# Kernel optimization log

Hardware: AMD Instinct MI355X
Metric: run time of the kernel (lower is better)

## Reference

```python
import jax, jax.numpy as jnp
import numpy as np

# Static multi-scale pyramid (H, W per level); Nv = sum(H*W) = 13294
SPATIAL = np.array([[100, 100], [50, 50], [25, 25], [13, 13]], dtype=np.int64)
B, C, NH, NL, NP = 2, 256, 8, 4, 4
D = C // NH
TOT = NH * NL * NP


def setup_inputs() -> dict:
    key = jax.random.key(0)
    ks = jax.random.split(key, 10)
    Nv = int((SPATIAL[:, 0] * SPATIAL[:, 1]).sum())
    Nq = Nv
    query = jax.random.normal(ks[0], (B, Nq, C), dtype=jnp.float32)
    value = jax.random.normal(ks[1], (B, Nv, C), dtype=jnp.float32)
    reference_points = jax.random.uniform(ks[2], (B, Nq, NL, 2), minval=0.05, maxval=0.95, dtype=jnp.float32)
    spatial_shapes = jnp.asarray(SPATIAL)
    level_start_index = jnp.asarray(np.concatenate([[0], np.cumsum(SPATIAL[:, 0] * SPATIAL[:, 1])[:-1]]))
    # sampling_offsets: small random weight + the rotated-grid bias from _reset_parameters
    W_off = 0.01 * jax.random.normal(ks[3], (C, TOT * 2), dtype=jnp.float32)
    thetas = np.arange(NH, dtype=np.float64) * (2.0 * np.pi / NH)
    grid = np.stack([np.cos(thetas), np.sin(thetas)], -1)
    grid = grid / np.abs(grid).max(-1, keepdims=True)
    grid = np.tile(grid[:, None, None, :], (1, NL, NP, 1)) * (np.arange(NP) + 1)[None, None, :, None]
    b_off = jnp.asarray(grid.reshape(-1), dtype=jnp.float32)
    W_attn = 0.01 * jax.random.normal(ks[4], (C, TOT), dtype=jnp.float32)
    b_attn = jnp.zeros((TOT,), jnp.float32)
    W_val = jax.random.normal(ks[5], (C, C), dtype=jnp.float32) / np.sqrt(C)
    b_val = jnp.zeros((C,), jnp.float32)
    W_out = jax.random.normal(ks[6], (C, C), dtype=jnp.float32) / np.sqrt(C)
    b_out = jnp.zeros((C,), jnp.float32)
    return {"query": query, "value": value, "reference_points": reference_points,
            "spatial_shapes": spatial_shapes, "level_start_index": level_start_index,
            "W_off": W_off, "b_off": b_off, "W_attn": W_attn, "b_attn": b_attn,
            "W_val": W_val, "b_val": b_val, "W_out": W_out, "b_out": b_out}


def _bilinear(vl, loc, H, W):
    # vl: [B, h, H*W, D]; loc: [B, Nq, h, P, 2] normalized (x, y) in [0,1]
    # Matches F.grid_sample(mode='bilinear', padding_mode='zeros', align_corners=False)
    Bb, h, _, Dd = vl.shape
    Nq, P = loc.shape[1], loc.shape[3]
    x = loc[..., 0] * W - 0.5
    y = loc[..., 1] * H - 0.5
    x0 = jnp.floor(x)
    y0 = jnp.floor(y)
    fx = x - x0
    fy = y - y0
    out = jnp.zeros((Bb, h, Nq * P, Dd), vl.dtype)
    corners = ((0, 0, (1 - fx) * (1 - fy)), (1, 0, fx * (1 - fy)),
               (0, 1, (1 - fx) * fy), (1, 1, fx * fy))
    for dx, dy, w in corners:
        xi = x0 + dx
        yi = y0 + dy
        valid = (xi >= 0) & (xi < W) & (yi >= 0) & (yi < H)
        idx = (jnp.clip(yi, 0, H - 1) * W + jnp.clip(xi, 0, W - 1)).astype(jnp.int32)
        idx = idx.transpose(0, 2, 1, 3).reshape(Bb, h, Nq * P)          # [B,h,Nq*P]
        wv = (w * valid).transpose(0, 2, 1, 3).reshape(Bb, h, Nq * P)   # [B,h,Nq*P]
        g = jnp.take_along_axis(vl, idx[..., None], axis=2)             # [B,h,Nq*P,D]
        out = out + g * wv[..., None]
    return out.reshape(Bb, h, Nq, P, Dd)


def reference(query, value, reference_points, spatial_shapes, level_start_index,
              W_off, b_off, W_attn, b_attn, W_val, b_val, W_out, b_out):
    Bb, Nq, Cc = query.shape
    v = (value @ W_val + b_val).reshape(Bb, -1, NH, D)                  # [B,Nv,h,D]
    off = (query @ W_off + b_off).reshape(Bb, Nq, NH, NL, NP, 2)
    attn = jax.nn.softmax((query @ W_attn + b_attn).reshape(Bb, Nq, NH, NL * NP), axis=-1)
    attn = attn.reshape(Bb, Nq, NH, NL, NP)
    # offset normalizer is (W, H) per level
    norm = jnp.asarray(SPATIAL[:, ::-1].copy(), dtype=query.dtype)      # [L,2]
    loc = reference_points[:, :, None, :, None, :] + off / norm[None, None, None, :, None, :]
    starts = np.concatenate([[0], np.cumsum(SPATIAL[:, 0] * SPATIAL[:, 1])])
    out_acc = jnp.zeros((Bb, NH, Nq, D), query.dtype)
    for l in range(NL):
        H, W = int(SPATIAL[l, 0]), int(SPATIAL[l, 1])
        vl = v[:, int(starts[l]):int(starts[l + 1])].transpose(0, 2, 1, 3)  # [B,h,HW,D]
        samp = _bilinear(vl, loc[:, :, :, l], H, W)                     # [B,h,Nq,P,D]
        w_l = attn[:, :, :, l].transpose(0, 2, 1, 3)                    # [B,h,Nq,P]
        out_acc = out_acc + jnp.einsum('bhqpd,bhqp->bhqd', samp, w_l)
    out = out_acc.transpose(0, 2, 1, 3).reshape(Bb, Nq, Cc)
    return out @ W_out + b_out
```

## Files before the change

kernel.cpp:

```cpp
#include <hip/hip_runtime.h>
#include <hip/hip_bf16.h>

#define NQ  13294
#define NV  13294
#define BQ  26588

typedef __attribute__((ext_vector_type(8))) short short8;
typedef __attribute__((ext_vector_type(4))) float f32x4;

static __device__ __forceinline__ ushort f2bf(float f) {
    unsigned int x = __float_as_uint(f);
    unsigned int r = (x + 0x7fffu + ((x >> 16) & 1u)) >> 16;
    return (ushort)r;
}
static __device__ __forceinline__ uint cvtpk_bf16(float a, float b) {
    uint r;
    asm("v_cvt_pk_bf16_f32 %0, %1, %2" : "=v"(r) : "v"(a), "v"(b));
    return r;
}
static __device__ __forceinline__ uint cvtpk_f16(float a, float b) {
    uint r;
    asm("v_cvt_pkrtz_f16_f32 %0, %1, %2" : "=v"(r) : "v"(a), "v"(b));
    return r;
}
static __device__ __forceinline__ float f16lo(uint u) {
    _Float16 h; ushort t = (ushort)(u & 0xffffu);
    __builtin_memcpy(&h, &t, 2); return (float)h;
}
static __device__ __forceinline__ float f16hi(uint u) {
    _Float16 h; ushort t = (ushort)(u >> 16);
    __builtin_memcpy(&h, &t, 2); return (float)h;
}
static __device__ __forceinline__ float fmamix_ll(float acc, uint g, uint w) {
    asm("v_fma_mix_f32 %0, %1, %2, %0 op_sel:[0,0,0] op_sel_hi:[1,1,0]" : "+v"(acc) : "v"(g), "v"(w));
    return acc;
}
static __device__ __forceinline__ float fmamix_hl(float acc, uint g, uint w) {
    asm("v_fma_mix_f32 %0, %1, %2, %0 op_sel:[1,0,0] op_sel_hi:[1,1,0]" : "+v"(acc) : "v"(g), "v"(w));
    return acc;
}
static __device__ __forceinline__ float fmamix_lh(float acc, uint g, uint w) {
    asm("v_fma_mix_f32 %0, %1, %2, %0 op_sel:[0,1,0] op_sel_hi:[1,1,0]" : "+v"(acc) : "v"(g), "v"(w));
    return acc;
}
static __device__ __forceinline__ float fmamix_hh(float acc, uint g, uint w) {
    asm("v_fma_mix_f32 %0, %1, %2, %0 op_sel:[1,1,0] op_sel_hi:[1,1,0]" : "+v"(acc) : "v"(g), "v"(w));
    return acc;
}

__global__ __launch_bounds__(256) void prep_weights(
    const float* __restrict__ Wv, const float* __restrict__ Wo,
    const float* __restrict__ Wa, const float* __restrict__ Wu,
    const float* __restrict__ bo, const float* __restrict__ ba,
    ushort* __restrict__ tWv, ushort* __restrict__ tWoa,
    ushort* __restrict__ tWu, float* __restrict__ boa) {
    const int blk = blockIdx.x;
    const int tid = threadIdx.x;
    if (blk == 56) {
        if (tid < 256) boa[tid] = bo[tid];
        int j = tid + 256;
        if (j < 384) boa[j] = ba[j - 256];
        return;
    }
    __shared__ float t[64][65];
    const float* src; ushort* dst; int srcN, k0, n0, drow0;
    if (blk < 16)      { int u = blk;      src = Wv; srcN = 256; dst = tWv;  k0 = (u >> 2) * 64; n0 = (u & 3) * 64; drow0 = n0; }
    else if (blk < 32) { int u = blk - 16; src = Wo; srcN = 256; dst = tWoa; k0 = (u >> 2) * 64; n0 = (u & 3) * 64; drow0 = n0; }
    else if (blk < 40) { int u = blk - 32; src = Wa; srcN = 128; dst = tWoa; k0 = (u >> 1) * 64; n0 = (u & 1) * 64; drow0 = 256 + n0; }
    else               { int u = blk - 40; src = Wu; srcN = 256; dst = tWu;  k0 = (u >> 2) * 64; n0 = (u & 3) * 64; drow0 = n0; }
#pragma unroll
    for (int it = 0; it < 16; ++it) {
        int idx = tid + it * 256, r = idx >> 6, c = idx & 63;
        t[r][c] = src[(size_t)(k0 + r) * srcN + n0 + c];
    }
    __syncthreads();
#pragma unroll
    for (int it = 0; it < 16; ++it) {
        int idx = tid + it * 256, r = idx >> 6, c = idx & 63;
        dst[(size_t)(drow0 + r) * 256 + k0 + c] = f2bf(t[c][r]);
    }
}

#define LDP 40

template<int AF32>
static __device__ __forceinline__ void gemm_core(
    const void* __restrict__ Aptr, const ushort* __restrict__ Bt,
    const float* __restrict__ bias, void* __restrict__ Cout,
    int M, int N, int out_mode, int mblk, int nblk,
    ushort* sA, ushort* sB) {
    const int tid = threadIdx.x;
    const int wid = tid >> 6;
    const int lane = tid & 63;
    const int row0 = mblk * 128;
    const int col0 = nblk * 128;
    const int wr = (wid >> 1) * 64;
    const int wc = (wid & 1) * 64;

    f32x4 acc[4][4];
#pragma unroll
    for (int m = 0; m < 4; ++m)
#pragma unroll
        for (int n = 0; n < 4; ++n) acc[m][n] = (f32x4){0.f, 0.f, 0.f, 0.f};

    for (int kk = 0; kk < 256; kk += 32) {
        __syncthreads();
#pragma unroll
        for (int it = 0; it < 2; ++it) {
            int chunk = tid + it * 256;
            int r = chunk >> 2;
            int seg = chunk & 3;
            int gr = row0 + r; gr = gr < M ? gr : M - 1;
            uint4 wa;
            if (AF32) {
                const float* Af = (const float*)Aptr + (size_t)gr * 256 + kk + seg * 8;
                float4 f0 = *reinterpret_cast<const float4*>(Af);
                float4 f1 = *reinterpret_cast<const float4*>(Af + 4);
                wa.x = cvtpk_bf16(f0.x, f0.y);
                wa.y = cvtpk_bf16(f0.z, f0.w);
                wa.z = cvtpk_bf16(f1.x, f1.y);
                wa.w = cvtpk_bf16(f1.z, f1.w);
            } else {
                wa = *reinterpret_cast<const uint4*>((const ushort*)Aptr + (size_t)gr * 256 + kk + seg * 8);
            }
            *reinterpret_cast<uint4*>(&sA[r * LDP + seg * 8]) = wa;
            int gc = col0 + r;
            uint4 vb4 = *reinterpret_cast<const uint4*>(Bt + (size_t)gc * 256 + kk + seg * 8);
            *reinterpret_cast<uint4*>(&sB[r * LDP + seg * 8]) = vb4;
        }
        __syncthreads();

        short8 a[4], b[4];
#pragma unroll
        for (int m = 0; m < 4; ++m)
            a[m] = *reinterpret_cast<const short8*>(&sA[(wr + m * 16 + (lane & 15)) * LDP + (lane >> 4) * 8]);
#pragma unroll
        for (int n = 0; n < 4; ++n)
            b[n] = *reinterpret_cast<const short8*>(&sB[(wc + n * 16 + (lane & 15)) * LDP + (lane >> 4) * 8]);
#pragma unroll
        for (int m = 0; m < 4; ++m)
#pragma unroll
            for (int n = 0; n < 4; ++n)
                acc[m][n] = __builtin_amdgcn_mfma_f32_16x16x32_bf16(a[m], b[n], acc[m][n], 0, 0, 0);
    }

    const int lr = (lane >> 4) * 4;
    const int lc = lane & 15;
#pragma unroll
    for (int m = 0; m < 4; ++m) {
#pragma unroll
        for (int n = 0; n < 4; ++n) {
            int gcol = col0 + wc + n * 16 + lc;
            float bv = bias[gcol];
#pragma unroll
            for (int j = 0; j < 4; ++j) {
                int grow = row0 + wr + m * 16 + lr + j;
                if (grow < M) {
                    float vv = acc[m][n][j] + bv;
                    if (out_mode == 0) {
                        ((float*)Cout)[(size_t)grow * N + gcol] = vv;
                    } else if (out_mode == 2) {
                        ((ushort*)Cout)[(size_t)grow * N + gcol] = (ushort)(cvtpk_f16(vv, vv) & 0xffffu);
                    } else {
                        int bb = grow >= NV;
                        int pix = grow - bb * NV;
                        int h = gcol >> 5, ch = gcol & 31;
                        ((ushort*)Cout)[(((size_t)(bb * 8 + h)) * NV + pix) * 32 + ch] =
                            (ushort)(cvtpk_f16(vv, vv) & 0xffffu);
                    }
                }
            }
        }
    }
}

__global__ __launch_bounds__(256) void gemm_fused(
    const float* __restrict__ value, const float* __restrict__ query,
    const ushort* __restrict__ tWv, const ushort* __restrict__ tWoa,
    const float* __restrict__ bval, const float* __restrict__ boa,
    ushort* __restrict__ vproj_t, ushort* __restrict__ offattn) {
    __shared__ ushort sA[128 * LDP];
    __shared__ ushort sB[128 * LDP];
    const bool g1 = blockIdx.y < 2;
    gemm_core<1>(g1 ? (const void*)value : (const void*)query,
                 g1 ? tWv : tWoa, g1 ? bval : boa,
                 g1 ? (void*)vproj_t : (void*)offattn,
                 BQ, g1 ? 256 : 384, g1 ? 3 : 2,
                 blockIdx.x, g1 ? blockIdx.y : blockIdx.y - 2, sA, sB);
}

__global__ __launch_bounds__(256) void gemm_out(
    const ushort* __restrict__ outacc, const ushort* __restrict__ tWu,
    const float* __restrict__ bout, float* __restrict__ dout) {
    __shared__ ushort sA[128 * LDP];
    __shared__ ushort sB[128 * LDP];
    gemm_core<0>(outacc, tWu, bout, dout, BQ, 256, 0, blockIdx.x, blockIdx.y, sA, sB);
}

__global__ __launch_bounds__(256, 4) void msda_sample(
    const ushort* __restrict__ offattn,
    const float* __restrict__ refp,
    const ushort* __restrict__ vt,
    ushort* __restrict__ out_acc) {
    __shared__ int2 s_ad[4][256];
    __shared__ uint s_w[4][256];

    const int tid = threadIdx.x;
    const int qi = tid >> 6;
    const int lane = tid & 63;
    const int bq = blockIdx.x * 4 + qi;
    const int b = bq / NQ;
    const int q = bq - b * NQ;
    const int h = lane >> 3;

    const ushort* oa = offattn + (size_t)bq * 384;
    const int t0 = lane * 2;
    uint lgu = *reinterpret_cast<const uint*>(oa + 256 + t0);
    float lg0 = f16lo(lgu), lg1 = f16hi(lgu);
    float m = fmaxf(lg0, lg1);
    m = fmaxf(m, __shfl_xor(m, 1));
    m = fmaxf(m, __shfl_xor(m, 2));
    m = fmaxf(m, __shfl_xor(m, 4));
    float e0 = __expf(lg0 - m), e1 = __expf(lg1 - m);
    float ssum = e0 + e1;
    ssum += __shfl_xor(ssum, 1);
    ssum += __shfl_xor(ssum, 2);
    ssum += __shfl_xor(ssum, 4);
    float inv = 1.f / ssum;

    uint2 offu = *reinterpret_cast<const uint2*>(oa + 2 * t0);
    const int l = (t0 >> 2) & 3;
    const int   Wi = (l == 0) ? 100 : (l == 1) ? 50 : (l == 2) ? 25 : 13;
    const int   st = (l == 0) ? 0 : (l == 1) ? 10000 : (l == 2) ? 12500 : 13125;
    const float Wf = (float)Wi;
    float rx = refp[(((size_t)b * NQ + q) * 4 + l) * 2 + 0];
    float ry = refp[(((size_t)b * NQ + q) * 4 + l) * 2 + 1];
    const int vbase = (b * 8 + h) * NV * 64;

#pragma unroll
    for (int j = 0; j < 2; ++j) {
        float e = (j ? e1 : e0) * inv;
        float ox = j ? f16lo(offu.y) : f16lo(offu.x);
        float oy = j ? f16hi(offu.y) : f16hi(offu.x);
        float x = fmaf(rx, Wf, ox) - 0.5f;
        float y = fmaf(ry, Wf, oy) - 0.5f;
        float x0f = floorf(x), y0f = floorf(y);
        float fx = x - x0f, fy = y - y0f;
        int x0 = (int)x0f, y0 = (int)y0f;
        float wx0 = (x0 >= 0 && x0 < Wi)         ? e * (1.f - fx) : 0.f;
        float wx1 = (x0 + 1 >= 0 && x0 + 1 < Wi) ? e * fx         : 0.f;
        float wy0 = (y0 >= 0 && y0 < Wi)         ? (1.f - fy) : 0.f;
        float wy1 = (y0 + 1 >= 0 && y0 + 1 < Wi) ? fy         : 0.f;
        int px0 = min(max(x0, 0), Wi - 1) * 64;
        int px1 = min(max(x0 + 1, 0), Wi - 1) * 64;
        int a0 = vbase + (st + min(max(y0, 0), Wi - 1) * Wi) * 64;
        int a1 = vbase + (st + min(max(y0 + 1, 0), Wi - 1) * Wi) * 64;
        int s = 2 * (lane & 7) + j;
        int u = ((s ^ h) << 4) + (h << 1);
        s_ad[qi][u]     = make_int2(a0 + px0, a1 + px0);
        s_ad[qi][u + 1] = make_int2(a0 + px1, a1 + px1);
        s_w[qi][u]      = cvtpk_f16(wx0 * wy0, wx0 * wy1);
        s_w[qi][u + 1]  = cvtpk_f16(wx1 * wy0, wx1 * wy1);
    }
    __syncthreads();

    const int xbit = (lane >> 2) & 1;
    const int cg16 = (lane & 3) * 16;
    const char* vtc = (const char*)vt;

    int2 A[16]; uint Wp[16];
#pragma unroll
    for (int ss = 0; ss < 16; ++ss) {
        int u = ((ss ^ h) << 4) + (h << 1) + xbit;
        int2 a = s_ad[qi][u];
        A[ss] = make_int2(a.x + cg16, a.y + cg16);
        Wp[ss] = s_w[qi][u];
    }

    float acc[8] = {0.f, 0.f, 0.f, 0.f, 0.f, 0.f, 0.f, 0.f};
#pragma unroll
    for (int ss = 0; ss < 16; ++ss) {
        uint4 g0 = *reinterpret_cast<const uint4*>(vtc + (uint)A[ss].x);
        uint4 g1 = *reinterpret_cast<const uint4*>(vtc + (uint)A[ss].y);
        uint w = Wp[ss];
        acc[0] = fmamix_ll(acc[0], g0.x, w); acc[1] = fmamix_hl(acc[1], g0.x, w);
        acc[2] = fmamix_ll(acc[2], g0.y, w); acc[3] = fmamix_hl(acc[3], g0.y, w);
        acc[4] = fmamix_ll(acc[4], g0.z, w); acc[5] = fmamix_hl(acc[5], g0.z, w);
        acc[6] = fmamix_ll(acc[6], g0.w, w); acc[7] = fmamix_hl(acc[7], g0.w, w);
        acc[0] = fmamix_lh(acc[0], g1.x, w); acc[1] = fmamix_hh(acc[1], g1.x, w);
        acc[2] = fmamix_lh(acc[2], g1.y, w); acc[3] = fmamix_hh(acc[3], g1.y, w);
        acc[4] = fmamix_lh(acc[4], g1.z, w); acc[5] = fmamix_hh(acc[5], g1.z, w);
        acc[6] = fmamix_lh(acc[6], g1.w, w); acc[7] = fmamix_hh(acc[7], g1.w, w);
    }

#pragma unroll
    for (int i = 0; i < 8; ++i) acc[i] += __shfl_xor(acc[i], 4);
    if (xbit == 0) {
        uint4 o;
        o.x = cvtpk_bf16(acc[0], acc[1]);
        o.y = cvtpk_bf16(acc[2], acc[3]);
        o.z = cvtpk_bf16(acc[4], acc[5]);
        o.w = cvtpk_bf16(acc[6], acc[7]);
        *reinterpret_cast<uint4*>(out_acc + (size_t)bq * 256 + h * 32 + (lane & 3) * 8) = o;
    }
}

extern "C" void kernel_launch(void* const* d_in, const int* in_sizes, int n_in,
                              void* d_out, int out_size, void* d_ws, size_t ws_size,
                              hipStream_t stream) {
    const float* query  = (const float*)d_in[0];
    const float* value  = (const float*)d_in[1];
    const float* refp   = (const float*)d_in[2];
    const float* W_off  = (const float*)d_in[5];
    const float* b_off  = (const float*)d_in[6];
    const float* W_attn = (const float*)d_in[7];
    const float* b_attn = (const float*)d_in[8];
    const float* W_val  = (const float*)d_in[9];
    const float* b_val  = (const float*)d_in[10];
    const float* W_out  = (const float*)d_in[11];
    const float* b_out  = (const float*)d_in[12];

    const size_t ROWB = (size_t)BQ * 256 * 2;
    char* ws = (char*)d_ws;
    ushort* vproj_t = (ushort*)(ws);
    ushort* outacc  = (ushort*)(ws + ROWB);
    ushort* offattn = (ushort*)(ws + 2 * ROWB);
    char*   wbase   = ws + 2 * ROWB + (size_t)BQ * 384 * 2;
    ushort* tWv  = (ushort*)(wbase);
    ushort* tWoa = tWv + 65536;
    ushort* tWu  = tWoa + 98304;
    float*  boa  = (float*)(tWu + 65536);

    prep_weights<<<57, 256, 0, stream>>>(
        W_val, W_off, W_attn, W_out, b_off, b_attn, tWv, tWoa, tWu, boa);

    gemm_fused<<<dim3(208, 5), 256, 0, stream>>>(
        value, query, tWv, tWoa, b_val, boa, vproj_t, offattn);

    msda_sample<<<BQ / 4, 256, 0, stream>>>(offattn, refp, vproj_t, outacc);

    gemm_out<<<dim3(208, 2), 256, 0, stream>>>(outacc, tWu, b_out, (float*)d_out);
}
```

Baseline: 107.9 us.

## Double-buffer GEMM shared-memory tiles with register prefetch of next K slice

The GEMM core now loads the next 32-wide K slice from global memory into registers while MFMAs run on the current shared-memory buffer. It then writes that slice into the alternate buffer, so each K step needs one barrier instead of two. This is meant to hide global-load latency behind compute in the projection GEMMs. In exchange it doubles LDS use per block, holds more prefetch registers, and adds a launch-bounds occupancy hint of 3 blocks per CU.

```diff
diff --git a/kernel.cpp b/kernel.cpp
--- a/kernel.cpp
+++ b/kernel.cpp
@@ -82,9 +82,10 @@
 }
 
 #define LDP 40
+#define ABUF (128 * LDP)
 
 template<int AF32>
-static __device__ __forceinline__ void gemm_core(
+static __device__ __forceinline__ void gemm_core2(
     const void* __restrict__ Aptr, const ushort* __restrict__ Bt,
     const float* __restrict__ bias, void* __restrict__ Cout,
     int M, int N, int out_mode, int mblk, int nblk,
@@ -103,45 +104,69 @@
 #pragma unroll
         for (int n = 0; n < 4; ++n) acc[m][n] = (f32x4){0.f, 0.f, 0.f, 0.f};
 
-    for (int kk = 0; kk < 256; kk += 32) {
-        __syncthreads();
+    const int r0 = tid >> 2;
+    const int seg = tid & 3;
+
+    float4 rf[4];
+    uint4  ra[2];
+    uint4  rb[2];
+
+    auto REGLOAD = [&](int kk) {
 #pragma unroll
         for (int it = 0; it < 2; ++it) {
-            int chunk = tid + it * 256;
-            int r = chunk >> 2;
-            int seg = chunk & 3;
+            int r = r0 + it * 64;
             int gr = row0 + r; gr = gr < M ? gr : M - 1;
+            if (AF32) {
+                const float* Af = (const float*)Aptr + (size_t)gr * 256 + kk + seg * 8;
+                rf[2 * it]     = *reinterpret_cast<const float4*>(Af);
+                rf[2 * it + 1] = *reinterpret_cast<const float4*>(Af + 4);
+            } else {
+                ra[it] = *reinterpret_cast<const uint4*>((const ushort*)Aptr + (size_t)gr * 256 + kk + seg * 8);
+            }
+            int gc = col0 + r;
+            rb[it] = *reinterpret_cast<const uint4*>(Bt + (size_t)gc * 256 + kk + seg * 8);
+        }
+    };
+    auto STORE = [&](int buf) {
+#pragma unroll
+        for (int it = 0; it < 2; ++it) {
+            int r = r0 + it * 64;
             uint4 wa;
             if (AF32) {
-                const float* Af = (const float*)Aptr + (size_t)gr * 256 + kk + seg * 8;
-                float4 f0 = *reinterpret_cast<const float4*>(Af);
-                float4 f1 = *reinterpret_cast<const float4*>(Af + 4);
-                wa.x = cvtpk_bf16(f0.x, f0.y);
-                wa.y = cvtpk_bf16(f0.z, f0.w);
-                wa.z = cvtpk_bf16(f1.x, f1.y);
-                wa.w = cvtpk_bf16(f1.z, f1.w);
+                wa.x = cvtpk_bf16(rf[2 * it].x, rf[2 * it].y);
+                wa.y = cvtpk_bf16(rf[2 * it].z, rf[2 * it].w);
+                wa.z = cvtpk_bf16(rf[2 * it + 1].x, rf[2 * it + 1].y);
+                wa.w = cvtpk_bf16(rf[2 * it + 1].z, rf[2 * it + 1].w);
             } else {
-                wa = *reinterpret_cast<const uint4*>((const ushort*)Aptr + (size_t)gr * 256 + kk + seg * 8);
+                wa = ra[it];
             }
-            *reinterpret_cast<uint4*>(&sA[r * LDP + seg * 8]) = wa;
-            int gc = col0 + r;
-            uint4 vb4 = *reinterpret_cast<const uint4*>(Bt + (size_t)gc * 256 + kk + seg * 8);
-            *reinterpret_cast<uint4*>(&sB[r * LDP + seg * 8]) = vb4;
+            *reinterpret_cast<uint4*>(&sA[buf * ABUF + r * LDP + seg * 8]) = wa;
+            *reinterpret_cast<uint4*>(&sB[buf * ABUF + r * LDP + seg * 8]) = rb[it];
         }
-        __syncthreads();
-
+    };
+    auto COMPUTE = [&](int buf) {
         short8 a[4], b[4];
 #pragma unroll
         for (int m = 0; m < 4; ++m)
-            a[m] = *reinterpret_cast<const short8*>(&sA[(wr + m * 16 + (lane & 15)) * LDP + (lane >> 4) * 8]);
+            a[m] = *reinterpret_cast<const short8*>(&sA[buf * ABUF + (wr + m * 16 + (lane & 15)) * LDP + (lane >> 4) * 8]);
 #pragma unroll
         for (int n = 0; n < 4; ++n)
-            b[n] = *reinterpret_cast<const short8*>(&sB[(wc + n * 16 + (lane & 15)) * LDP + (lane >> 4) * 8]);
+            b[n] = *reinterpret_cast<const short8*>(&sB[buf * ABUF + (wc + n * 16 + (lane & 15)) * LDP + (lane >> 4) * 8]);
 #pragma unroll
         for (int m = 0; m < 4; ++m)
 #pragma unroll
             for (int n = 0; n < 4; ++n)
                 acc[m][n] = __builtin_amdgcn_mfma_f32_16x16x32_bf16(a[m], b[n], acc[m][n], 0, 0, 0);
+    };
+
+    REGLOAD(0);
+    STORE(0);
+#pragma unroll
+    for (int t = 0; t < 8; ++t) {
+        __syncthreads();
+        if (t < 7) REGLOAD((t + 1) * 32);
+        COMPUTE(t & 1);
+        if (t < 7) STORE((t + 1) & 1);
     }
 
     const int lr = (lane >> 4) * 4;
@@ -174,27 +199,27 @@
     }
 }
 
-__global__ __launch_bounds__(256) void gemm_fused(
+__global__ __launch_bounds__(256, 3) void gemm_fused(
     const float* __restrict__ value, const float* __restrict__ query,
     const ushort* __restrict__ tWv, const ushort* __restrict__ tWoa,
     const float* __restrict__ bval, const float* __restrict__ boa,
     ushort* __restrict__ vproj_t, ushort* __restrict__ offattn) {
-    __shared__ ushort sA[128 * LDP];
-    __shared__ ushort sB[128 * LDP];
+    __shared__ ushort sA[2 * ABUF];
+    __shared__ ushort sB[2 * ABUF];
     const bool g1 = blockIdx.y < 2;
-    gemm_core<1>(g1 ? (const void*)value : (const void*)query,
-                 g1 ? tWv : tWoa, g1 ? bval : boa,
-                 g1 ? (void*)vproj_t : (void*)offattn,
-                 BQ, g1 ? 256 : 384, g1 ? 3 : 2,
-                 blockIdx.x, g1 ? blockIdx.y : blockIdx.y - 2, sA, sB);
-}
-
-__global__ __launch_bounds__(256) void gemm_out(
+    gemm_core2<1>(g1 ? (const void*)value : (const void*)query,
+                  g1 ? tWv : tWoa, g1 ? bval : boa,
+                  g1 ? (void*)vproj_t : (void*)offattn,
+                  BQ, g1 ? 256 : 384, g1 ? 3 : 2,
+                  blockIdx.x, g1 ? blockIdx.y : blockIdx.y - 2, sA, sB);
+}
+
+__global__ __launch_bounds__(256, 3) void gemm_out(
     const ushort* __restrict__ outacc, const ushort* __restrict__ tWu,
     const float* __restrict__ bout, float* __restrict__ dout) {
-    __shared__ ushort sA[128 * LDP];
-    __shared__ ushort sB[128 * LDP];
-    gemm_core<0>(outacc, tWu, bout, dout, BQ, 256, 0, blockIdx.x, blockIdx.y, sA, sB);
+    __shared__ ushort sA[2 * ABUF];
+    __shared__ ushort sB[2 * ABUF];
+    gemm_core2<0>(outacc, tWu, bout, dout, BQ, 256, 0, blockIdx.x, blockIdx.y, sA, sB);
 }
 
 __global__ __launch_bounds__(256, 4) void msda_sample(
```

Result: no change. 107.8 us (-0.0%).

## Keep full-K A row panel resident in LDS and loop over N blocks

Applied to the files above, without the earlier changes.

GEMMs now load a 128-row A panel for the whole K=256 into shared memory once (converting fp32 to bf16 once) and iterate over all N column blocks inside one block. B tiles are register-prefetched one K step ahead. This removes repeated global reads and conversions of A across column blocks, at the cost of fewer blocks, larger dynamic LDS per block and serialized N work.

```diff
diff --git a/kernel.cpp b/kernel.cpp
--- a/kernel.cpp
+++ b/kernel.cpp
@@ -7,6 +7,10 @@
 
 typedef __attribute__((ext_vector_type(8))) short short8;
 typedef __attribute__((ext_vector_type(4))) float f32x4;
+
+#define ALD 264
+#define BLD 40
+#define LDS_USH (128 * ALD + 128 * BLD)
 
 static __device__ __forceinline__ ushort f2bf(float f) {
     unsigned int x = __float_as_uint(f);
@@ -81,92 +85,109 @@
     }
 }
 
-#define LDP 40
-
 template<int AF32>
-static __device__ __forceinline__ void gemm_core(
+static __device__ __forceinline__ void gemm_rowres(
     const void* __restrict__ Aptr, const ushort* __restrict__ Bt,
     const float* __restrict__ bias, void* __restrict__ Cout,
-    int M, int N, int out_mode, int mblk, int nblk,
-    ushort* sA, ushort* sB) {
+    int M, int N, int out_mode, int mblk, ushort* sA, ushort* sB) {
     const int tid = threadIdx.x;
     const int wid = tid >> 6;
     const int lane = tid & 63;
     const int row0 = mblk * 128;
-    const int col0 = nblk * 128;
     const int wr = (wid >> 1) * 64;
     const int wc = (wid & 1) * 64;
 
-    f32x4 acc[4][4];
-#pragma unroll
-    for (int m = 0; m < 4; ++m)
-#pragma unroll
-        for (int n = 0; n < 4; ++n) acc[m][n] = (f32x4){0.f, 0.f, 0.f, 0.f};
-
-    for (int kk = 0; kk < 256; kk += 32) {
-        __syncthreads();
-#pragma unroll
-        for (int it = 0; it < 2; ++it) {
-            int chunk = tid + it * 256;
-            int r = chunk >> 2;
-            int seg = chunk & 3;
+    if (AF32) {
+        const float* Af = (const float*)Aptr;
+#pragma unroll 8
+        for (int it = 0; it < 32; ++it) {
+            int idx = tid + it * 256;
+            int r = idx >> 6, c4 = idx & 63;
             int gr = row0 + r; gr = gr < M ? gr : M - 1;
-            uint4 wa;
-            if (AF32) {
-                const float* Af = (const float*)Aptr + (size_t)gr * 256 + kk + seg * 8;
-                float4 f0 = *reinterpret_cast<const float4*>(Af);
-                float4 f1 = *reinterpret_cast<const float4*>(Af + 4);
-                wa.x = cvtpk_bf16(f0.x, f0.y);
-                wa.y = cvtpk_bf16(f0.z, f0.w);
-                wa.z = cvtpk_bf16(f1.x, f1.y);
-                wa.w = cvtpk_bf16(f1.z, f1.w);
-            } else {
-                wa = *reinterpret_cast<const uint4*>((const ushort*)Aptr + (size_t)gr * 256 + kk + seg * 8);
-            }
-            *reinterpret_cast<uint4*>(&sA[r * LDP + seg * 8]) = wa;
-            int gc = col0 + r;
-            uint4 vb4 = *reinterpret_cast<const uint4*>(Bt + (size_t)gc * 256 + kk + seg * 8);
-            *reinterpret_cast<uint4*>(&sB[r * LDP + seg * 8]) = vb4;
+            float4 f = *reinterpret_cast<const float4*>(Af + (size_t)gr * 256 + c4 * 4);
+            uint2 w;
+            w.x = cvtpk_bf16(f.x, f.y);
+            w.y = cvtpk_bf16(f.z, f.w);
+            *reinterpret_cast<uint2*>(&sA[r * ALD + c4 * 4]) = w;
         }
-        __syncthreads();
-
-        short8 a[4], b[4];
+    } else {
+        const ushort* Ab = (const ushort*)Aptr;
+#pragma unroll 8
+        for (int it = 0; it < 16; ++it) {
+            int idx = tid + it * 256;
+            int r = idx >> 5, c = idx & 31;
+            int gr = row0 + r; gr = gr < M ? gr : M - 1;
+            uint4 v = *reinterpret_cast<const uint4*>(Ab + (size_t)gr * 256 + c * 8);
+            *reinterpret_cast<uint4*>(&sA[r * ALD + c * 8]) = v;
+        }
+    }
+
+    const int rbase = lane & 15;
+    const int kseg = (lane >> 4) * 8;
+    const int brow = tid >> 2;
+    const int bseg = (tid & 3) * 8;
+
+    const int nNB = N >> 7;
+    for (int nb = 0; nb < nNB; ++nb) {
+        const int col0 = nb * 128;
+        f32x4 acc[4][4];
 #pragma unroll
         for (int m = 0; m < 4; ++m)
-            a[m] = *reinterpret_cast<const short8*>(&sA[(wr + m * 16 + (lane & 15)) * LDP + (lane >> 4) * 8]);
-#pragma unroll
-        for (int n = 0; n < 4; ++n)
-            b[n] = *reinterpret_cast<const short8*>(&sB[(wc + n * 16 + (lane & 15)) * LDP + (lane >> 4) * 8]);
-#pragma unroll
-        for (int m = 0; m < 4; ++m)
+#pragma unroll
+            for (int n = 0; n < 4; ++n) acc[m][n] = (f32x4){0.f, 0.f, 0.f, 0.f};
+
+        uint4 rb0, rb1;
+        auto LOADB = [&](int kk) {
+            rb0 = *reinterpret_cast<const uint4*>(Bt + (size_t)(col0 + brow) * 256 + kk + bseg);
+            rb1 = *reinterpret_cast<const uint4*>(Bt + (size_t)(col0 + brow + 64) * 256 + kk + bseg);
+        };
+        LOADB(0);
+#pragma unroll
+        for (int t = 0; t < 8; ++t) {
+            __syncthreads();
+            *reinterpret_cast<uint4*>(&sB[brow * BLD + bseg]) = rb0;
+            *reinterpret_cast<uint4*>(&sB[(brow + 64) * BLD + bseg]) = rb1;
+            __syncthreads();
+            if (t < 7) LOADB((t + 1) * 32);
+            const int kk = t * 32;
+            short8 a[4], b[4];
+#pragma unroll
+            for (int m = 0; m < 4; ++m)
+                a[m] = *reinterpret_cast<const short8*>(&sA[(wr + m * 16 + rbase) * ALD + kk + kseg]);
 #pragma unroll
             for (int n = 0; n < 4; ++n)
-                acc[m][n] = __builtin_amdgcn_mfma_f32_16x16x32_bf16(a[m], b[n], acc[m][n], 0, 0, 0);
-    }
-
-    const int lr = (lane >> 4) * 4;
-    const int lc = lane & 15;
-#pragma unroll
-    for (int m = 0; m < 4; ++m) {
-#pragma unroll
-        for (int n = 0; n < 4; ++n) {
-            int gcol = col0 + wc + n * 16 + lc;
-            float bv = bias[gcol];
-#pragma unroll
-            for (int j = 0; j < 4; ++j) {
-                int grow = row0 + wr + m * 16 + lr + j;
-                if (grow < M) {
-                    float vv = acc[m][n][j] + bv;
-                    if (out_mode == 0) {
-                        ((float*)Cout)[(size_t)grow * N + gcol] = vv;
-                    } else if (out_mode == 2) {
-                        ((ushort*)Cout)[(size_t)grow * N + gcol] = (ushort)(cvtpk_f16(vv, vv) & 0xffffu);
-                    } else {
-                        int bb = grow >= NV;
-                        int pix = grow - bb * NV;
-                        int h = gcol >> 5, ch = gcol & 31;
-                        ((ushort*)Cout)[(((size_t)(bb * 8 + h)) * NV + pix) * 32 + ch] =
-                            (ushort)(cvtpk_f16(vv, vv) & 0xffffu);
+                b[n] = *reinterpret_cast<const short8*>(&sB[(wc + n * 16 + rbase) * BLD + kseg]);
+#pragma unroll
+            for (int m = 0; m < 4; ++m)
+#pragma unroll
+                for (int n = 0; n < 4; ++n)
+                    acc[m][n] = __builtin_amdgcn_mfma_f32_16x16x32_bf16(a[m], b[n], acc[m][n], 0, 0, 0);
+        }
+
+        const int lr = (lane >> 4) * 4;
+        const int lc = lane & 15;
+#pragma unroll
+        for (int m = 0; m < 4; ++m) {
+#pragma unroll
+            for (int n = 0; n < 4; ++n) {
+                int gcol = col0 + wc + n * 16 + lc;
+                float bv = bias[gcol];
+#pragma unroll
+                for (int j = 0; j < 4; ++j) {
+                    int grow = row0 + wr + m * 16 + lr + j;
+                    if (grow < M) {
+                        float vv = acc[m][n][j] + bv;
+                        if (out_mode == 0) {
+                            ((float*)Cout)[(size_t)grow * N + gcol] = vv;
+                        } else if (out_mode == 2) {
+                            ((ushort*)Cout)[(size_t)grow * N + gcol] = (ushort)(cvtpk_f16(vv, vv) & 0xffffu);
+                        } else {
+                            int bb = grow >= NV;
+                            int pix = grow - bb * NV;
+                            int h = gcol >> 5, ch = gcol & 31;
+                            ((ushort*)Cout)[(((size_t)(bb * 8 + h)) * NV + pix) * 32 + ch] =
+                                (ushort)(cvtpk_f16(vv, vv) & 0xffffu);
+                        }
                     }
                 }
             }
@@ -174,27 +195,27 @@
     }
 }
 
-__global__ __launch_bounds__(256) void gemm_fused(
+__global__ __launch_bounds__(256) void gemm_big(
     const float* __restrict__ value, const float* __restrict__ query,
     const ushort* __restrict__ tWv, const ushort* __restrict__ tWoa,
     const float* __restrict__ bval, const float* __restrict__ boa,
     ushort* __restrict__ vproj_t, ushort* __restrict__ offattn) {
-    __shared__ ushort sA[128 * LDP];
-    __shared__ ushort sB[128 * LDP];
-    const bool g1 = blockIdx.y < 2;
-    gemm_core<1>(g1 ? (const void*)value : (const void*)query,
-                 g1 ? tWv : tWoa, g1 ? bval : boa,
-                 g1 ? (void*)vproj_t : (void*)offattn,
-                 BQ, g1 ? 256 : 384, g1 ? 3 : 2,
-                 blockIdx.x, g1 ? blockIdx.y : blockIdx.y - 2, sA, sB);
-}
-
-__global__ __launch_bounds__(256) void gemm_out(
+    extern __shared__ ushort smem[];
+    ushort* sA = smem;
+    ushort* sB = smem + 128 * ALD;
+    if (blockIdx.y == 0)
+        gemm_rowres<1>(value, tWv, bval, vproj_t, BQ, 256, 3, blockIdx.x, sA, sB);
+    else
+        gemm_rowres<1>(query, tWoa, boa, offattn, BQ, 384, 2, blockIdx.x, sA, sB);
+}
+
+__global__ __launch_bounds__(256) void gemm_out2(
     const ushort* __restrict__ outacc, const ushort* __restrict__ tWu,
     const float* __restrict__ bout, float* __restrict__ dout) {
-    __shared__ ushort sA[128 * LDP];
-    __shared__ ushort sB[128 * LDP];
-    gemm_core<0>(outacc, tWu, bout, dout, BQ, 256, 0, blockIdx.x, blockIdx.y, sA, sB);
+    extern __shared__ ushort smem[];
+    ushort* sA = smem;
+    ushort* sB = smem + 128 * ALD;
+    gemm_rowres<0>(outacc, tWu, bout, dout, BQ, 256, 0, blockIdx.x, sA, sB);
 }
 
 __global__ __launch_bounds__(256, 4) void msda_sample(
@@ -331,13 +352,15 @@
     ushort* tWu  = tWoa + 98304;
     float*  boa  = (float*)(tWu + 65536);
 
+    const size_t DLDS = (size_t)LDS_USH * 2;
+
     prep_weights<<<57, 256, 0, stream>>>(
         W_val, W_off, W_attn, W_out, b_off, b_attn, tWv, tWoa, tWu, boa);
 
-    gemm_fused<<<dim3(208, 5), 256, 0, stream>>>(
+    gemm_big<<<dim3(208, 2), 256, DLDS, stream>>>(
         value, query, tWv, tWoa, b_val, boa, vproj_t, offattn);
 
     msda_sample<<<BQ / 4, 256, 0, stream>>>(offattn, refp, vproj_t, outacc);
 
-    gemm_out<<<dim3(208, 2), 256, 0, stream>>>(outacc, tWu, b_out, (float*)d_out);
-}
+    gemm_out2<<<208, 256, DLDS, stream>>>(outacc, tWu, b_out, (float*)d_out);
+}
```

After: 117.9 us. 1.09x slower.
